# Optimization experiments

Measured on AMD Instinct MI355X. Metric: run time of the kernel, lower is better.

The kernel has to match this reference:

```python
import jax, jax.numpy as jnp
import numpy as np

H = 256  # num_hidden

def setup_inputs() -> dict:
    key = jax.random.key(0)
    k1, k2, k3 = jax.random.split(key, 3)
    B, S, V = 256, 512, 128
    tokens = jax.random.randint(k1, (B, S), 0, V, dtype=jnp.int32)
    emb = jax.random.normal(k2, (V, H), dtype=jnp.float32)
    # Fused gate weights for the four Linear(2H -> H) layers: order [i, f, o, u]
    W = jax.random.normal(k3, (2 * H, 4 * H), dtype=jnp.float32) * (1.0 / np.sqrt(2 * H))
    b = jnp.zeros((4 * H,), dtype=jnp.float32)
    return {"tokens": tokens, "emb": emb, "W": W, "b": b}

def reference(tokens, emb, W, b):
    # tokens: [B, S] int; emb: [V, H]; W: [2H, 4H]; b: [4H]
    x = emb[tokens]                      # [B, S, H] gathered embeddings
    B = x.shape[0]
    h0 = jnp.zeros((B, H), dtype=x.dtype)
    c0 = jnp.zeros((B, H), dtype=x.dtype)

    def step(carry, xt):
        h, c = carry
        z = jnp.concatenate([h, xt], axis=-1) @ W + b   # [B, 4H]
        i = jax.nn.sigmoid(z[:, 0 * H:1 * H])           # 'data' gate
        f = jax.nn.sigmoid(z[:, 1 * H:2 * H])           # 'forget' gate
        o = jax.nn.sigmoid(z[:, 2 * H:3 * H])           # 'output' gate
        u = jnp.tanh(z[:, 3 * H:4 * H])                 # 'input' candidate
        c_new = i * u + f * c
        h_new = o * jnp.tanh(c_new)
        return (h_new, c_new), h_new

    (_, _), hs = jax.lax.scan(step, (h0, c0), jnp.swapaxes(x, 0, 1))  # hs: [S, B, H]
    return jnp.swapaxes(hs, 0, 1)  # [B, S, H]
```

## Files before the change

### kernel.cpp

```cpp
#include <hip/hip_runtime.h>
#include <hip/hip_bf16.h>


#define HID    256
#define FOURH  1024
#define SLEN   512
#define NVOCAB 128
#define BSZ    16

typedef __attribute__((ext_vector_type(8))) __bf16 bf16x8;
typedef __attribute__((ext_vector_type(4))) float  f32x4;

__device__ __forceinline__ unsigned short f2bf(float x) {
  unsigned int u = __builtin_bit_cast(unsigned int, x);
  u = (u + 0x7FFFu + ((u >> 16) & 1u)) >> 16;
  return (unsigned short)u;
}
__device__ __forceinline__ float sigmoid_(float x) {
  return __builtin_amdgcn_rcpf(1.f + __expf(-x));
}
__device__ __forceinline__ float tanh_(float x) {
  return 1.f - 2.f * __builtin_amdgcn_rcpf(__expf(2.f * x) + 1.f);
}

__global__ __launch_bounds__(256) void lstm_prep(
    const float* __restrict__ emb, const float* __restrict__ W,
    const float* __restrict__ b, float* __restrict__ zx,
    unsigned short* __restrict__ Wb)
{
  const int blk = blockIdx.x;
  if (blk < NVOCAB) {
    __shared__ float ev[HID];
    const int v = blk;
    for (int i = threadIdx.x; i < HID; i += 256) ev[i] = emb[v * HID + i];
    __syncthreads();
    for (int jj = 0; jj < 4; ++jj) {
      const int col = jj * 256 + threadIdx.x;
      float acc = b[col];
      #pragma unroll 4
      for (int k = 0; k < HID; ++k)
        acc += ev[k] * W[(HID + k) * FOURH + col];
      zx[v * FOURH + col] = acc;
    }
  } else {
    int idx = (blk - NVOCAB) * 256 + threadIdx.x;
    const int c = idx >> 9;
    const int rem = idx & 511;
    const int s = rem >> 6, gg = (rem >> 4) & 3, r = rem & 15;
    const int col = 16 * c + r;
    #pragma unroll
    for (int j = 0; j < 8; ++j) {
      const int k = 32 * s + 8 * gg + j;
      Wb[(((c * 8 + s) * 4 + gg) * 16 + r) * 8 + j] = f2bf(W[k * FOURH + col]);
    }
  }
}

__global__ __launch_bounds__(1024, 4) void lstm_seq(
    const int* __restrict__ tokens, const float* __restrict__ zx,
    const unsigned short* __restrict__ Wb, float* __restrict__ out)
{
  __shared__ __align__(16) unsigned short hbuf[2][4096];
  const int tid = threadIdx.x;
  const int w = tid >> 6, l = tid & 63;
  const int g = l >> 4, r = l & 15;
  const int b0 = blockIdx.x * BSZ;
  const int row4 = 4 * g;

  for (int i = tid; i < 2 * 4096; i += 1024) ((unsigned short*)hbuf)[i] = 0;

  bf16x8 wf[32];
  const unsigned short* wl = Wb + (size_t)l * 8;
  #pragma unroll
  for (int q = 0; q < 4; ++q)
    #pragma unroll
    for (int s = 0; s < 8; ++s)
      wf[q * 8 + s] = *reinterpret_cast<const bf16x8*>(
          wl + (size_t)(16 * q + w) * 4096 + s * 512);

  float cst[4] = {0.f, 0.f, 0.f, 0.f};

  const int colw = 16 * w + r;
  const int s4 = colw >> 5, gg = (colw >> 3) & 3, jj = colw & 7;

  __syncthreads();

  for (int t = 0; t < SLEN; ++t) {
    const int pp = t & 1;

    int tok[4];
    #pragma unroll
    for (int j = 0; j < 4; ++j)
      tok[j] = tokens[(b0 + row4 + j) * SLEN + t];
    float zxv[4][4];
    #pragma unroll
    for (int j = 0; j < 4; ++j) {
      const float* zp = zx + (size_t)tok[j] * FOURH + colw;
      #pragma unroll
      for (int q = 0; q < 4; ++q) zxv[q][j] = zp[q * 256];
    }

    bf16x8 a[8];
    #pragma unroll
    for (int s = 0; s < 8; ++s)
      a[s] = *reinterpret_cast<const bf16x8*>(&hbuf[pp][(s * 64 + l) * 8]);

    f32x4 acc[4];
    #pragma unroll
    for (int q = 0; q < 4; ++q) {
      f32x4 A = {0.f, 0.f, 0.f, 0.f};
      #pragma unroll
      for (int s = 0; s < 8; ++s)
        A = __builtin_amdgcn_mfma_f32_16x16x32_bf16(a[s], wf[q * 8 + s], A, 0, 0, 0);
      acc[q] = A;
    }

    #pragma unroll
    for (int j = 0; j < 4; ++j) {
      const float zi = acc[0][j] + zxv[0][j];
      const float zf = acc[1][j] + zxv[1][j];
      const float zo = acc[2][j] + zxv[2][j];
      const float zu = acc[3][j] + zxv[3][j];
      const float iv = sigmoid_(zi);
      const float fv = sigmoid_(zf);
      const float ov = sigmoid_(zo);
      const float uv = tanh_(zu);
      const float cn = iv * uv + fv * cst[j];
      cst[j] = cn;
      const float hn = ov * tanh_(cn);
      out[(size_t)(b0 + row4 + j) * (SLEN * HID) + (size_t)t * HID + colw] = hn;
      hbuf[pp ^ 1][((s4 * 4 + gg) * 16 + (row4 + j)) * 8 + jj] = f2bf(hn);
    }
    __syncthreads();
  }
}

extern "C" void kernel_launch(void* const* d_in, const int* in_sizes, int n_in,
                              void* d_out, int out_size, void* d_ws, size_t ws_size,
                              hipStream_t stream) {
  const int*   tokens = (const int*)d_in[0];
  const float* emb    = (const float*)d_in[1];
  const float* W      = (const float*)d_in[2];
  const float* b      = (const float*)d_in[3];
  float* out = (float*)d_out;

  float*          zx = (float*)d_ws;
  unsigned short* Wb = (unsigned short*)((char*)d_ws + 512 * 1024);

  lstm_prep<<<256, 256, 0, stream>>>(emb, W, b, zx, Wb);
  lstm_seq<<<16, 1024, 0, stream>>>(tokens, zx, Wb, out);
}
```

Baseline: 3.700 ms.

## Prefetch next-step input projections with gate-interleaved layout and nontemporal output stores

The precomputed input projection table is reordered so the four gate values for a column sit together, which lets each thread fetch them with a single 16-byte load. The load for step t+1 is issued before step t's MFMA work so its latency overlaps the compute. Output writes become nontemporal stores through incrementing pointers. Launch bounds are relaxed to one block per SM and the weight fragments are pinned in registers with an asm barrier, which raises register pressure but keeps the weights resident.

```diff
diff --git a/kernel.cpp b/kernel.cpp
--- a/kernel.cpp
+++ b/kernel.cpp
@@ -25,7 +25,7 @@
 
 __global__ __launch_bounds__(256) void lstm_prep(
     const float* __restrict__ emb, const float* __restrict__ W,
-    const float* __restrict__ b, float* __restrict__ zx,
+    const float* __restrict__ b, float* __restrict__ zx2,
     unsigned short* __restrict__ Wb)
 {
   const int blk = blockIdx.x;
@@ -34,13 +34,13 @@
     const int v = blk;
     for (int i = threadIdx.x; i < HID; i += 256) ev[i] = emb[v * HID + i];
     __syncthreads();
-    for (int jj = 0; jj < 4; ++jj) {
-      const int col = jj * 256 + threadIdx.x;
+    for (int q = 0; q < 4; ++q) {
+      const int col = q * 256 + threadIdx.x;
       float acc = b[col];
       #pragma unroll 4
       for (int k = 0; k < HID; ++k)
         acc += ev[k] * W[(HID + k) * FOURH + col];
-      zx[v * FOURH + col] = acc;
+      zx2[((size_t)v * 256 + threadIdx.x) * 4 + q] = acc;
     }
   } else {
     int idx = (blk - NVOCAB) * 256 + threadIdx.x;
@@ -56,8 +56,8 @@
   }
 }
 
-__global__ __launch_bounds__(1024, 4) void lstm_seq(
-    const int* __restrict__ tokens, const float* __restrict__ zx,
+__global__ __launch_bounds__(1024, 1) void lstm_seq(
+    const int* __restrict__ tokens, const float* __restrict__ zx2,
     const unsigned short* __restrict__ Wb, float* __restrict__ out)
 {
   __shared__ __align__(16) unsigned short hbuf[2][4096];
@@ -69,35 +69,48 @@
 
   for (int i = tid; i < 2 * 4096; i += 1024) ((unsigned short*)hbuf)[i] = 0;
 
-  bf16x8 wf[32];
+  f32x4 wf[32];
   const unsigned short* wl = Wb + (size_t)l * 8;
   #pragma unroll
   for (int q = 0; q < 4; ++q)
     #pragma unroll
     for (int s = 0; s < 8; ++s)
-      wf[q * 8 + s] = *reinterpret_cast<const bf16x8*>(
+      wf[q * 8 + s] = *reinterpret_cast<const f32x4*>(
           wl + (size_t)(16 * q + w) * 4096 + s * 512);
+  #pragma unroll
+  for (int i = 0; i < 32; ++i) asm volatile("" : "+v"(wf[i]));
 
   float cst[4] = {0.f, 0.f, 0.f, 0.f};
 
   const int colw = 16 * w + r;
   const int s4 = colw >> 5, gg = (colw >> 3) & 3, jj = colw & 7;
 
+  const int* trp[4];
+  float* op[4];
+  #pragma unroll
+  for (int j = 0; j < 4; ++j) {
+    trp[j] = tokens + (size_t)(b0 + row4 + j) * SLEN;
+    op[j]  = out + (size_t)(b0 + row4 + j) * (SLEN * HID) + colw;
+  }
+
+  f32x4 zxc[4];
+  #pragma unroll
+  for (int j = 0; j < 4; ++j) {
+    const int tk = trp[j][0];
+    zxc[j] = *reinterpret_cast<const f32x4*>(zx2 + ((size_t)tk * 256 + colw) * 4);
+  }
+
   __syncthreads();
 
   for (int t = 0; t < SLEN; ++t) {
     const int pp = t & 1;
 
-    int tok[4];
-    #pragma unroll
-    for (int j = 0; j < 4; ++j)
-      tok[j] = tokens[(b0 + row4 + j) * SLEN + t];
-    float zxv[4][4];
+    const int tn = (t + 1 < SLEN) ? t + 1 : SLEN - 1;
+    f32x4 zxn[4];
     #pragma unroll
     for (int j = 0; j < 4; ++j) {
-      const float* zp = zx + (size_t)tok[j] * FOURH + colw;
-      #pragma unroll
-      for (int q = 0; q < 4; ++q) zxv[q][j] = zp[q * 256];
+      const int tk = trp[j][tn];
+      zxn[j] = *reinterpret_cast<const f32x4*>(zx2 + ((size_t)tk * 256 + colw) * 4);
     }
 
     bf16x8 a[8];
@@ -111,16 +124,17 @@
       f32x4 A = {0.f, 0.f, 0.f, 0.f};
       #pragma unroll
       for (int s = 0; s < 8; ++s)
-        A = __builtin_amdgcn_mfma_f32_16x16x32_bf16(a[s], wf[q * 8 + s], A, 0, 0, 0);
+        A = __builtin_amdgcn_mfma_f32_16x16x32_bf16(
+            a[s], __builtin_bit_cast(bf16x8, wf[q * 8 + s]), A, 0, 0, 0);
       acc[q] = A;
     }
 
     #pragma unroll
     for (int j = 0; j < 4; ++j) {
-      const float zi = acc[0][j] + zxv[0][j];
-      const float zf = acc[1][j] + zxv[1][j];
-      const float zo = acc[2][j] + zxv[2][j];
-      const float zu = acc[3][j] + zxv[3][j];
+      const float zi = acc[0][j] + zxc[j][0];
+      const float zf = acc[1][j] + zxc[j][1];
+      const float zo = acc[2][j] + zxc[j][2];
+      const float zu = acc[3][j] + zxc[j][3];
       const float iv = sigmoid_(zi);
       const float fv = sigmoid_(zf);
       const float ov = sigmoid_(zo);
@@ -128,9 +142,14 @@
       const float cn = iv * uv + fv * cst[j];
       cst[j] = cn;
       const float hn = ov * tanh_(cn);
-      out[(size_t)(b0 + row4 + j) * (SLEN * HID) + (size_t)t * HID + colw] = hn;
+      __builtin_nontemporal_store(hn, op[j]);
+      op[j] += HID;
       hbuf[pp ^ 1][((s4 * 4 + gg) * 16 + (row4 + j)) * 8 + jj] = f2bf(hn);
     }
+
+    #pragma unroll
+    for (int j = 0; j < 4; ++j) zxc[j] = zxn[j];
+
     __syncthreads();
   }
 }
@@ -144,9 +163,9 @@
   const float* b      = (const float*)d_in[3];
   float* out = (float*)d_out;
 
-  float*          zx = (float*)d_ws;
-  unsigned short* Wb = (unsigned short*)((char*)d_ws + 512 * 1024);
+  float*          zx2 = (float*)d_ws;
+  unsigned short* Wb  = (unsigned short*)((char*)d_ws + 512 * 1024);
 
-  lstm_prep<<<256, 256, 0, stream>>>(emb, W, b, zx, Wb);
-  lstm_seq<<<16, 1024, 0, stream>>>(tokens, zx, Wb, out);
+  lstm_prep<<<256, 256, 0, stream>>>(emb, W, b, zx2, Wb);
+  lstm_seq<<<16, 1024, 0, stream>>>(tokens, zx2, Wb, out);
 }
```

Measured after the change: 4.193 ms. 1.13x slower.

## Split LSTM hidden columns across 8 cooperating blocks with global-flag exchange

Applied to the files above, without the earlier changes.

The sequential kernel goes from 16 blocks of 1024 threads to 128 blocks of 512 threads. Each group of 8 blocks shares one 16-row batch slice, and each block owns a 32-column slice of the hidden state. Each step, a block writes its new h slice to a global double-buffered exchange, sets a per-block release flag, spins until all 8 peers reach the step, then gathers the full h into LDS. This spreads the recurrence over more CUs and holds fewer weights per wave, and the next step's zx is prefetched with a reordered layout. The cost is a cross-block global synchronisation every timestep. It also relies on all 128 blocks being co-resident, otherwise it deadlocks, and it adds a dummy LDS pad that appears meant to limit occupancy.

```diff
diff --git a/kernel.cpp b/kernel.cpp
--- a/kernel.cpp
+++ b/kernel.cpp
@@ -6,10 +6,10 @@
 #define FOURH  1024
 #define SLEN   512
 #define NVOCAB 128
-#define BSZ    16
 
 typedef __attribute__((ext_vector_type(8))) __bf16 bf16x8;
 typedef __attribute__((ext_vector_type(4))) float  f32x4;
+typedef unsigned long long ull;
 
 __device__ __forceinline__ unsigned short f2bf(float x) {
   unsigned int u = __builtin_bit_cast(unsigned int, x);
@@ -25,22 +25,24 @@
 
 __global__ __launch_bounds__(256) void lstm_prep(
     const float* __restrict__ emb, const float* __restrict__ W,
-    const float* __restrict__ b, float* __restrict__ zx,
-    unsigned short* __restrict__ Wb)
+    const float* __restrict__ b, float* __restrict__ zxs,
+    unsigned short* __restrict__ Wb, unsigned int* __restrict__ flags)
 {
   const int blk = blockIdx.x;
   if (blk < NVOCAB) {
+    if (blk == 0 && threadIdx.x < 128) flags[threadIdx.x] = 0;
     __shared__ float ev[HID];
     const int v = blk;
     for (int i = threadIdx.x; i < HID; i += 256) ev[i] = emb[v * HID + i];
     __syncthreads();
-    for (int jj = 0; jj < 4; ++jj) {
-      const int col = jj * 256 + threadIdx.x;
+    const int jj = threadIdx.x >> 5, cloc = threadIdx.x & 31;
+    for (int q = 0; q < 4; ++q) {
+      const int col = q * 256 + threadIdx.x;
       float acc = b[col];
       #pragma unroll 4
       for (int k = 0; k < HID; ++k)
         acc += ev[k] * W[(HID + k) * FOURH + col];
-      zx[v * FOURH + col] = acc;
+      zxs[(((size_t)v * 8 + jj) * 32 + cloc) * 4 + q] = acc;
     }
   } else {
     int idx = (blk - NVOCAB) * 256 + threadIdx.x;
@@ -56,81 +58,110 @@
   }
 }
 
-__global__ __launch_bounds__(1024, 4) void lstm_seq(
-    const int* __restrict__ tokens, const float* __restrict__ zx,
-    const unsigned short* __restrict__ Wb, float* __restrict__ out)
+__global__ __launch_bounds__(512, 2) void lstm_seq(
+    const int* __restrict__ tokens, const float* __restrict__ zxs,
+    const unsigned short* __restrict__ Wb, ull* xbuf,
+    unsigned int* flags, float* __restrict__ out)
 {
-  __shared__ __align__(16) unsigned short hbuf[2][4096];
+  __shared__ __align__(16) unsigned short hbuf[4096];
+  __shared__ float zbuf[4][16][33];
+  __shared__ ull lpad[8320];
+
   const int tid = threadIdx.x;
   const int w = tid >> 6, l = tid & 63;
-  const int g = l >> 4, r = l & 15;
-  const int b0 = blockIdx.x * BSZ;
-  const int row4 = 4 * g;
+  const int q = w & 3, hc = w >> 2;
+  const int gid = blockIdx.x >> 3, j = blockIdx.x & 7;
+  const int b0 = gid * 16;
+  const int ctile = q * 16 + j * 2 + hc;
 
-  for (int i = tid; i < 2 * 4096; i += 1024) ((unsigned short*)hbuf)[i] = 0;
+  if (tokens[0] == -2147483647) lpad[tid] = 0;
 
-  bf16x8 wf[32];
-  const unsigned short* wl = Wb + (size_t)l * 8;
+  bf16x8 wf[8];
   #pragma unroll
-  for (int q = 0; q < 4; ++q)
-    #pragma unroll
-    for (int s = 0; s < 8; ++s)
-      wf[q * 8 + s] = *reinterpret_cast<const bf16x8*>(
-          wl + (size_t)(16 * q + w) * 4096 + s * 512);
+  for (int s = 0; s < 8; ++s)
+    wf[s] = *reinterpret_cast<const bf16x8*>(
+        Wb + (size_t)ctile * 4096 + s * 512 + l * 8);
+  #pragma unroll
+  for (int s = 0; s < 8; ++s) asm volatile("" : "+v"(wf[s]));
 
-  float cst[4] = {0.f, 0.f, 0.f, 0.f};
+  for (int i = tid; i < 1024; i += 512) reinterpret_cast<ull*>(hbuf)[i] = 0;
 
-  const int colw = 16 * w + r;
-  const int s4 = colw >> 5, gg = (colw >> 3) & 3, jj = colw & 7;
+  const int gr = tid >> 5, gc = tid & 31;
+  float cst = 0.f;
+  ull* xg = xbuf + (size_t)gid * 2048;
+  unsigned int* fg = flags + gid * 8;
 
   __syncthreads();
 
+  int tok0 = tokens[(b0 + gr) * SLEN];
+  f32x4 zxc = *reinterpret_cast<const f32x4*>(
+      &zxs[(((size_t)tok0 * 8 + j) * 32 + gc) * 4]);
+
+  unsigned int tgt = 1;
+  #pragma unroll 1
   for (int t = 0; t < SLEN; ++t) {
-    const int pp = t & 1;
-
-    int tok[4];
-    #pragma unroll
-    for (int j = 0; j < 4; ++j)
-      tok[j] = tokens[(b0 + row4 + j) * SLEN + t];
-    float zxv[4][4];
-    #pragma unroll
-    for (int j = 0; j < 4; ++j) {
-      const float* zp = zx + (size_t)tok[j] * FOURH + colw;
-      #pragma unroll
-      for (int q = 0; q < 4; ++q) zxv[q][j] = zp[q * 256];
-    }
+    const int tn = (t + 1 < SLEN) ? t + 1 : SLEN - 1;
+    const int tokn = tokens[(b0 + gr) * SLEN + tn];
+    const f32x4 zxn = *reinterpret_cast<const f32x4*>(
+        &zxs[(((size_t)tokn * 8 + j) * 32 + gc) * 4]);
 
     bf16x8 a[8];
     #pragma unroll
     for (int s = 0; s < 8; ++s)
-      a[s] = *reinterpret_cast<const bf16x8*>(&hbuf[pp][(s * 64 + l) * 8]);
+      a[s] = *reinterpret_cast<const bf16x8*>(&hbuf[(s * 64 + l) * 8]);
 
-    f32x4 acc[4];
+    f32x4 A = {0.f, 0.f, 0.f, 0.f};
     #pragma unroll
-    for (int q = 0; q < 4; ++q) {
-      f32x4 A = {0.f, 0.f, 0.f, 0.f};
-      #pragma unroll
-      for (int s = 0; s < 8; ++s)
-        A = __builtin_amdgcn_mfma_f32_16x16x32_bf16(a[s], wf[q * 8 + s], A, 0, 0, 0);
-      acc[q] = A;
+    for (int s = 0; s < 8; ++s)
+      A = __builtin_amdgcn_mfma_f32_16x16x32_bf16(a[s], wf[s], A, 0, 0, 0);
+    #pragma unroll
+    for (int p = 0; p < 4; ++p)
+      zbuf[q][4 * (l >> 4) + p][hc * 16 + (l & 15)] = A[p];
+    __syncthreads();
+
+    const float zi = zbuf[0][gr][gc] + zxc[0];
+    const float zf = zbuf[1][gr][gc] + zxc[1];
+    const float zo = zbuf[2][gr][gc] + zxc[2];
+    const float zu = zbuf[3][gr][gc] + zxc[3];
+    const float iv = sigmoid_(zi);
+    const float fv = sigmoid_(zf);
+    const float ov = sigmoid_(zo);
+    const float uv = tanh_(zu);
+    const float cn = iv * uv + fv * cst;
+    cst = cn;
+    const float hn = ov * tanh_(cn);
+    out[(size_t)(b0 + gr) * (SLEN * HID) + (size_t)t * HID + j * 32 + gc] = hn;
+    zxc = zxn;
+
+    const unsigned hu = (unsigned)f2bf(hn);
+    const unsigned v01 = hu | ((unsigned)__shfl_down((int)hu, 1) << 16);
+    const ull vch = (ull)v01 | ((ull)(unsigned)__shfl_down((int)v01, 2) << 32);
+    const int slot = t & 1;
+    if ((tid & 3) == 0) {
+      const int m = (tid >> 2) & 7;
+      __hip_atomic_store(&xg[(slot * 8 + j) * 128 + gr * 8 + m], vch,
+                         __ATOMIC_RELAXED, __HIP_MEMORY_SCOPE_AGENT);
     }
+    __syncthreads();
+    if (tid == 0)
+      __hip_atomic_store(&fg[j], tgt, __ATOMIC_RELEASE, __HIP_MEMORY_SCOPE_AGENT);
+
+    if (tid < 8) {
+      while (__hip_atomic_load(&fg[tid], __ATOMIC_RELAXED,
+                               __HIP_MEMORY_SCOPE_AGENT) < tgt) {}
+    }
+    __syncthreads();
+    __builtin_amdgcn_fence(__ATOMIC_ACQUIRE, "agent");
 
     #pragma unroll
-    for (int j = 0; j < 4; ++j) {
-      const float zi = acc[0][j] + zxv[0][j];
-      const float zf = acc[1][j] + zxv[1][j];
-      const float zo = acc[2][j] + zxv[2][j];
-      const float zu = acc[3][j] + zxv[3][j];
-      const float iv = sigmoid_(zi);
-      const float fv = sigmoid_(zf);
-      const float ov = sigmoid_(zo);
-      const float uv = tanh_(zu);
-      const float cn = iv * uv + fv * cst[j];
-      cst[j] = cn;
-      const float hn = ov * tanh_(cn);
-      out[(size_t)(b0 + row4 + j) * (SLEN * HID) + (size_t)t * HID + colw] = hn;
-      hbuf[pp ^ 1][((s4 * 4 + gg) * 16 + (row4 + j)) * 8 + jj] = f2bf(hn);
+    for (int n = tid; n < 1024; n += 512) {
+      const int p = n >> 7, rem = n & 127, r = rem >> 3, m = rem & 7;
+      const ull v = __hip_atomic_load(&xg[(slot * 8 + p) * 128 + rem],
+                                      __ATOMIC_RELAXED, __HIP_MEMORY_SCOPE_AGENT);
+      *reinterpret_cast<ull*>(
+          &hbuf[((p * 4 + (m >> 1)) * 16 + r) * 8 + (m & 1) * 4]) = v;
     }
+    ++tgt;
     __syncthreads();
   }
 }
@@ -144,9 +175,11 @@
   const float* b      = (const float*)d_in[3];
   float* out = (float*)d_out;
 
-  float*          zx = (float*)d_ws;
-  unsigned short* Wb = (unsigned short*)((char*)d_ws + 512 * 1024);
+  float*          zxs   = (float*)d_ws;
+  unsigned short* Wb    = (unsigned short*)((char*)d_ws + 512 * 1024);
+  ull*            xbuf  = (ull*)((char*)d_ws + 1024 * 1024);
+  unsigned int*   flags = (unsigned int*)((char*)d_ws + 1280 * 1024);
 
-  lstm_prep<<<256, 256, 0, stream>>>(emb, W, b, zx, Wb);
-  lstm_seq<<<16, 1024, 0, stream>>>(tokens, zx, Wb, out);
+  lstm_prep<<<256, 256, 0, stream>>>(emb, W, b, zxs, Wb, flags);
+  lstm_seq<<<128, 512, 0, stream>>>(tokens, zxs, Wb, xbuf, flags, out);
 }
```

New measurement: 5.438 ms. 1.47x slower.
